# Performance work log

Measured on AMD Instinct MI355X. Metric: run time of the kernel, lower is better.

Reference implementation:

```python
import jax, jax.numpy as jnp
import numpy as np

B, M, C, D, H, W = 2, 4, 32, 32, 32, 32
E, O = 4, 128
MC = M * C
BN_EPS = 1e-5


def setup_inputs() -> dict:
    key = jax.random.key(0)
    ks = jax.random.split(key, 8)
    inp = {
        "f0": jax.random.normal(ks[0], (B, C, D, H, W), jnp.float32),
        "f1": jax.random.normal(ks[1], (B, C, D, H, W), jnp.float32),
        "f2": jax.random.normal(ks[2], (B, C, D, H, W), jnp.float32),
        "f3": jax.random.normal(ks[3], (B, C, D, H, W), jnp.float32),
        # per-expert 1x1x1 conv weights [E, O, MC] (bias=False)
        "Wc": jax.random.normal(ks[4], (E, O, MC), jnp.float32) * 0.05,
        # BatchNorm3d params (eval mode), per expert per out-channel
        "gamma": jnp.ones((E, O), jnp.float32),
        "beta": jnp.zeros((E, O), jnp.float32),
        "rmean": jnp.zeros((E, O), jnp.float32),
        "rvar": jnp.ones((E, O), jnp.float32),
        # router Linear(MC -> E)
        "Wr": jax.random.normal(ks[5], (E, MC), jnp.float32) * 0.02,
        "br": jnp.zeros((E,), jnp.float32),
        "top_k": 2,
    }
    return inp


def reference(f0, f1, f2, f3, Wc, gamma, beta, rmean, rvar, Wr, br, top_k):
    x = jnp.concatenate([f0, f1, f2, f3], axis=1)          # [B, MC, D, H, W]
    Bn, MCn, Dn, Hn, Wn = x.shape
    En = Wr.shape[0]

    # router: global average pool -> linear -> softmax -> top-k
    pooled = x.mean(axis=(2, 3, 4))                        # [B, MC]
    logits = pooled @ Wr.T + br                            # [B, E]
    probs = jax.nn.softmax(logits, axis=-1)
    topk_vals, topk_idx = jax.lax.top_k(probs, top_k)      # [B, k]
    topk_w = topk_vals / topk_vals.sum(axis=-1, keepdims=True)

    # auxiliary load-balancing loss (top-1 one-hot)
    one_hot = jax.nn.one_hot(topk_idx[:, 0], En, dtype=probs.dtype)
    f_e = one_hot.mean(axis=0)
    p_e = probs.mean(axis=0)
    aux_loss = En * (f_e * p_e).sum()

    # all experts: 1x1x1 conv == channel GEMM, then eval-mode BN + ReLU
    xs = x.reshape(Bn, MCn, -1)                            # [B, MC, S]
    y = jnp.einsum('eoc,bcs->ebos', Wc, xs)                # [E, B, O, S]
    inv = gamma * jax.lax.rsqrt(rvar + BN_EPS)             # [E, O]
    y = y * inv[:, None, :, None] + (beta - rmean * inv)[:, None, :, None]
    y = jax.nn.relu(y)

    # dispatch/combine: per-sample expert weights scattered to [B, E]
    cw = jnp.zeros((Bn, En), x.dtype).at[
        jnp.arange(Bn)[:, None], topk_idx
    ].add(topk_w)
    out = jnp.einsum('be,ebos->bos', cw, y).reshape(Bn, -1, Dn, Hn, Wn)
    return out, aux_loss
```

## Files before the change

### kernel.cpp

```cpp
#include <hip/hip_runtime.h>
#include <stdint.h>

#define S_TOT 32768
#define MC_DIM 128
#define O_DIM 128
#define BN_EPS 1e-5f
#define S_TILE 128

#define WS_PART  0
#define WS_BIAS  512
#define WS_W2    1024

typedef __attribute__((ext_vector_type(8))) short short8;
typedef __attribute__((ext_vector_type(4))) float f32x4;

static __device__ __forceinline__ unsigned short f2bf(float f) {
    union { float f; unsigned int u; } v; v.f = f;
    unsigned int r = v.u + 0x7FFFu + ((v.u >> 16) & 1u);
    return (unsigned short)(r >> 16);
}

__global__ __launch_bounds__(256) void k_pool(
    const float* __restrict__ f0, const float* __restrict__ f1,
    const float* __restrict__ f2, const float* __restrict__ f3,
    const float* __restrict__ Wc, const float* __restrict__ gamma,
    const float* __restrict__ beta, const float* __restrict__ rmean,
    const float* __restrict__ rvar, float* __restrict__ ws) {

    __shared__ float red[4];
    int bid = blockIdx.x;
    int b = bid >> 7, c = bid & 127;
    int t = threadIdx.x;
    int wv = t >> 6, l = t & 63;

    if (t < 64) {
        int i = bid * 64 + t;
        int eo = i >> 5;
        float inv = gamma[eo] * rsqrtf(rvar[eo] + BN_EPS);
        float4 w = ((const float4*)Wc)[i];
        uint2 pk;
        pk.x = (unsigned int)f2bf(w.x * inv) | ((unsigned int)f2bf(w.y * inv) << 16);
        pk.y = (unsigned int)f2bf(w.z * inv) | ((unsigned int)f2bf(w.w * inv) << 16);
        ((uint2*)(ws + WS_W2))[i] = pk;
    } else if (t < 66) {
        int i = bid * 2 + (t - 64);
        float inv = gamma[i] * rsqrtf(rvar[i] + BN_EPS);
        ws[WS_BIAS + i] = beta[i] - rmean[i] * inv;
    }

    const float* fp = (c < 32) ? f0 : (c < 64) ? f1 : (c < 96) ? f2 : f3;
    const float4* base = (const float4*)(fp + ((size_t)b * 32 + (c & 31)) * S_TOT);
    float s = 0.f;
    #pragma unroll
    for (int j = 0; j < 32; ++j) {
        float4 v = base[j * 256 + t];
        s += (v.x + v.y) + (v.z + v.w);
    }
    #pragma unroll
    for (int msk = 32; msk >= 1; msk >>= 1) s += __shfl_xor(s, msk);
    if (l == 0) red[wv] = s;
    __syncthreads();
    if (t == 0) ws[WS_PART + bid] = (red[0] + red[1]) + (red[2] + red[3]);
}

__global__ __launch_bounds__(256, 2) void k_moe(
    const float* __restrict__ f0, const float* __restrict__ f1,
    const float* __restrict__ f2, const float* __restrict__ f3,
    const float* __restrict__ Wr, const float* __restrict__ br,
    const float* __restrict__ ws, float* __restrict__ out) {

    __shared__ uint4 tile4[2048];
    char* lds = (char*)tile4;

    int bid = blockIdx.x;
    int b = bid >> 8;
    int st = bid & 255;
    int s0 = st * S_TILE;
    int t = threadIdx.x;
    int wv = t >> 6, l = t & 63;

    float lg[8];
    {
        float p0 = ws[WS_PART + l];
        float p1 = ws[WS_PART + 64 + l];
        float p2 = ws[WS_PART + 128 + l];
        float p3 = ws[WS_PART + 192 + l];
        #pragma unroll
        for (int e = 0; e < 4; ++e) {
            float wc0 = Wr[e * MC_DIM + l];
            float wc1 = Wr[e * MC_DIM + 64 + l];
            lg[e]     = p0 * wc0 + p1 * wc1;
            lg[4 + e] = p2 * wc0 + p3 * wc1;
        }
        #pragma unroll
        for (int msk = 32; msk >= 1; msk >>= 1) {
            #pragma unroll
            for (int e = 0; e < 8; ++e) lg[e] += __shfl_xor(lg[e], msk);
        }
    }
    int e0, e1;
    float w0, w1;
    {
        const float s_inv = 1.0f / (float)S_TOT;
        float probs[2][4];
        int top1[2];
        int ee0[2], ee1[2];
        float vv0[2], vv1[2];
        #pragma unroll
        for (int bb = 0; bb < 2; ++bb) {
            float lo[4];
            #pragma unroll
            for (int e = 0; e < 4; ++e) lo[e] = lg[bb * 4 + e] * s_inv + br[e];
            float mx = fmaxf(fmaxf(lo[0], lo[1]), fmaxf(lo[2], lo[3]));
            float sum = 0.f;
            #pragma unroll
            for (int e = 0; e < 4; ++e) { probs[bb][e] = __expf(lo[e] - mx); sum += probs[bb][e]; }
            float rs = 1.f / sum;
            #pragma unroll
            for (int e = 0; e < 4; ++e) probs[bb][e] *= rs;
            int a0 = 0; float m0 = probs[bb][0];
            #pragma unroll
            for (int e = 1; e < 4; ++e) if (probs[bb][e] > m0) { m0 = probs[bb][e]; a0 = e; }
            int a1 = -1; float m1 = -1.f;
            #pragma unroll
            for (int e = 0; e < 4; ++e) if (e != a0 && probs[bb][e] > m1) { m1 = probs[bb][e]; a1 = e; }
            top1[bb] = a0; ee0[bb] = a0; ee1[bb] = a1; vv0[bb] = m0; vv1[bb] = m1;
        }
        float inv = 1.f / (vv0[b] + vv1[b]);
        e0 = ee0[b]; e1 = ee1[b];
        w0 = vv0[b] * inv; w1 = vv1[b] * inv;
        if (bid == 0 && t == 0) {
            float aux = 0.f;
            #pragma unroll
            for (int e = 0; e < 4; ++e) {
                float fe = 0.5f * ((top1[0] == e) + (top1[1] == e));
                float pe = 0.5f * (probs[0][e] + probs[1][e]);
                aux += fe * pe;
            }
            out[(size_t)8388608] = 4.f * aux;
        }
    }

    #pragma unroll
    for (int m = 0; m < 4; ++m) {
        const float* fp = (m == 0) ? f0 : (m == 1) ? f1 : (m == 2) ? f2 : f3;
        #pragma unroll
        for (int it = 0; it < 4; ++it) {
            int lin = it * 256 + t;
            int cql = lin >> 7;
            int sl = lin & 127;
            const float* src = fp + ((size_t)b * 32 + cql * 4) * S_TOT + s0 + sl;
            float v0 = src[0];
            float v1 = src[S_TOT];
            float v2 = src[2 * (size_t)S_TOT];
            float v3 = src[3 * (size_t)S_TOT];
            int cq = m * 8 + cql;
            int gr = cq >> 1, half = cq & 1;
            int gswz = gr ^ (sl & 15);
            int byte = sl * 256 + gswz * 16 + half * 8;
            uint2 pk;
            pk.x = (unsigned int)f2bf(v0) | ((unsigned int)f2bf(v1) << 16);
            pk.y = (unsigned int)f2bf(v2) | ((unsigned int)f2bf(v3) << 16);
            *(uint2*)(lds + byte) = pk;
        }
    }
    __syncthreads();

    const unsigned short* W2 = (const unsigned short*)(ws + WS_W2);
    const float* bias2 = ws + WS_BIAS;

    int o0 = wv * 32;
    int lr = l & 15, lg2 = l >> 4;

    f32x4 acc[2][2][8];
    #pragma unroll
    for (int ee = 0; ee < 2; ++ee)
        #pragma unroll
        for (int of = 0; of < 2; ++of)
            #pragma unroll
            for (int sf = 0; sf < 8; ++sf)
                acc[ee][of][sf] = (f32x4){0.f, 0.f, 0.f, 0.f};

    #pragma unroll
    for (int kk = 0; kk < 4; ++kk) {
        short8 a[2][2];
        #pragma unroll
        for (int ee = 0; ee < 2; ++ee) {
            int e = ee ? e1 : e0;
            #pragma unroll
            for (int of = 0; of < 2; ++of) {
                int o = o0 + of * 16 + lr;
                a[ee][of] = *(const short8*)(W2 + ((size_t)(e * O_DIM + o) * MC_DIM + kk * 32 + lg2 * 8));
            }
        }
        #pragma unroll
        for (int sf = 0; sf < 8; ++sf) {
            int sl = sf * 16 + lr;
            int gr = kk * 4 + lg2;
            int byte = sl * 256 + ((gr ^ lr) << 4);
            short8 bb = *(const short8*)(lds + byte);
            #pragma unroll
            for (int ee = 0; ee < 2; ++ee)
                #pragma unroll
                for (int of = 0; of < 2; ++of)
                    acc[ee][of][sf] = __builtin_amdgcn_mfma_f32_16x16x32_bf16(
                        a[ee][of], bb, acc[ee][of][sf], 0, 0, 0);
        }
    }

    #pragma unroll
    for (int of = 0; of < 2; ++of) {
        #pragma unroll
        for (int r = 0; r < 4; ++r) {
            int o = o0 + of * 16 + lg2 * 4 + r;
            float bA = bias2[e0 * O_DIM + o];
            float bB = bias2[e1 * O_DIM + o];
            float* orow = out + ((size_t)(b * O_DIM + o)) * S_TOT + s0;
            #pragma unroll
            for (int sf = 0; sf < 8; ++sf) {
                float y0 = fmaxf(acc[0][of][sf][r] + bA, 0.f);
                float y1 = fmaxf(acc[1][of][sf][r] + bB, 0.f);
                orow[sf * 16 + lr] = w0 * y0 + w1 * y1;
            }
        }
    }
}

extern "C" void kernel_launch(void* const* d_in, const int* in_sizes, int n_in,
                              void* d_out, int out_size, void* d_ws, size_t ws_size,
                              hipStream_t stream) {
    const float* f0    = (const float*)d_in[0];
    const float* f1    = (const float*)d_in[1];
    const float* f2    = (const float*)d_in[2];
    const float* f3    = (const float*)d_in[3];
    const float* Wc    = (const float*)d_in[4];
    const float* gamma = (const float*)d_in[5];
    const float* beta  = (const float*)d_in[6];
    const float* rmean = (const float*)d_in[7];
    const float* rvar  = (const float*)d_in[8];
    const float* Wr    = (const float*)d_in[9];
    const float* br    = (const float*)d_in[10];
    float* ws  = (float*)d_ws;
    float* out = (float*)d_out;

    hipLaunchKernelGGL(k_pool, dim3(256), dim3(256), 0, stream,
                       f0, f1, f2, f3, Wc, gamma, beta, rmean, rvar, ws);
    hipLaunchKernelGGL(k_moe, dim3(512), dim3(256), 0, stream,
                       f0, f1, f2, f3, Wr, br, ws, out);
}
```

Baseline: 27.95 us.

## Split pooling across two halves and use 256-wide spatial tiles with 512 threads

The pooling kernel now splits each channel's spatial reduction across two blocks (512 blocks in total), and the MoE kernel sums the two partial results. The MoE kernel doubles its spatial tile to 256 and uses 512-thread blocks in which each wave owns 16 output channels instead of 32, halving the grid to 256 blocks. The aim is more parallelism in the bandwidth-bound pool pass and fewer, larger GEMM blocks that reuse the weight fragments over more spatial columns. In exchange, LDS doubles to 64KB per block and the grid drops to 256 blocks, which may leave CUs idle or lower occupancy.

```diff
diff --git a/kernel.cpp b/kernel.cpp
--- a/kernel.cpp
+++ b/kernel.cpp
@@ -5,7 +5,7 @@
 #define MC_DIM 128
 #define O_DIM 128
 #define BN_EPS 1e-5f
-#define S_TILE 128
+#define S_TILE 256
 
 #define WS_PART  0
 #define WS_BIAS  512
@@ -29,12 +29,13 @@
 
     __shared__ float red[4];
     int bid = blockIdx.x;
-    int b = bid >> 7, c = bid & 127;
+    int half = bid >> 8, ch = bid & 255;
+    int b = ch >> 7, c = ch & 127;
     int t = threadIdx.x;
     int wv = t >> 6, l = t & 63;
 
-    if (t < 64) {
-        int i = bid * 64 + t;
+    if (t < 32) {
+        int i = bid * 32 + t;
         int eo = i >> 5;
         float inv = gamma[eo] * rsqrtf(rvar[eo] + BN_EPS);
         float4 w = ((const float4*)Wc)[i];
@@ -42,17 +43,16 @@
         pk.x = (unsigned int)f2bf(w.x * inv) | ((unsigned int)f2bf(w.y * inv) << 16);
         pk.y = (unsigned int)f2bf(w.z * inv) | ((unsigned int)f2bf(w.w * inv) << 16);
         ((uint2*)(ws + WS_W2))[i] = pk;
-    } else if (t < 66) {
-        int i = bid * 2 + (t - 64);
-        float inv = gamma[i] * rsqrtf(rvar[i] + BN_EPS);
-        ws[WS_BIAS + i] = beta[i] - rmean[i] * inv;
+    } else if (t == 32) {
+        float inv = gamma[bid] * rsqrtf(rvar[bid] + BN_EPS);
+        ws[WS_BIAS + bid] = beta[bid] - rmean[bid] * inv;
     }
 
     const float* fp = (c < 32) ? f0 : (c < 64) ? f1 : (c < 96) ? f2 : f3;
-    const float4* base = (const float4*)(fp + ((size_t)b * 32 + (c & 31)) * S_TOT);
+    const float4* base = (const float4*)(fp + ((size_t)b * 32 + (c & 31)) * S_TOT + half * 16384);
     float s = 0.f;
     #pragma unroll
-    for (int j = 0; j < 32; ++j) {
+    for (int j = 0; j < 16; ++j) {
         float4 v = base[j * 256 + t];
         s += (v.x + v.y) + (v.z + v.w);
     }
@@ -60,31 +60,31 @@
     for (int msk = 32; msk >= 1; msk >>= 1) s += __shfl_xor(s, msk);
     if (l == 0) red[wv] = s;
     __syncthreads();
-    if (t == 0) ws[WS_PART + bid] = (red[0] + red[1]) + (red[2] + red[3]);
-}
-
-__global__ __launch_bounds__(256, 2) void k_moe(
+    if (t == 0) ws[WS_PART + half * 256 + ch] = (red[0] + red[1]) + (red[2] + red[3]);
+}
+
+__global__ __launch_bounds__(512, 1) void k_moe(
     const float* __restrict__ f0, const float* __restrict__ f1,
     const float* __restrict__ f2, const float* __restrict__ f3,
     const float* __restrict__ Wr, const float* __restrict__ br,
     const float* __restrict__ ws, float* __restrict__ out) {
 
-    __shared__ uint4 tile4[2048];
+    __shared__ uint4 tile4[4096];
     char* lds = (char*)tile4;
 
     int bid = blockIdx.x;
-    int b = bid >> 8;
-    int st = bid & 255;
+    int b = bid >> 7;
+    int st = bid & 127;
     int s0 = st * S_TILE;
     int t = threadIdx.x;
     int wv = t >> 6, l = t & 63;
 
     float lg[8];
     {
-        float p0 = ws[WS_PART + l];
-        float p1 = ws[WS_PART + 64 + l];
-        float p2 = ws[WS_PART + 128 + l];
-        float p3 = ws[WS_PART + 192 + l];
+        float p0 = ws[WS_PART + l]       + ws[WS_PART + 256 + l];
+        float p1 = ws[WS_PART + 64 + l]  + ws[WS_PART + 320 + l];
+        float p2 = ws[WS_PART + 128 + l] + ws[WS_PART + 384 + l];
+        float p3 = ws[WS_PART + 192 + l] + ws[WS_PART + 448 + l];
         #pragma unroll
         for (int e = 0; e < 4; ++e) {
             float wc0 = Wr[e * MC_DIM + l];
@@ -146,9 +146,9 @@
         const float* fp = (m == 0) ? f0 : (m == 1) ? f1 : (m == 2) ? f2 : f3;
         #pragma unroll
         for (int it = 0; it < 4; ++it) {
-            int lin = it * 256 + t;
-            int cql = lin >> 7;
-            int sl = lin & 127;
+            int lin = it * 512 + t;
+            int cql = lin >> 8;
+            int sl = lin & 255;
             const float* src = fp + ((size_t)b * 32 + cql * 4) * S_TOT + s0 + sl;
             float v0 = src[0];
             float v1 = src[S_TOT];
@@ -169,59 +169,49 @@
     const unsigned short* W2 = (const unsigned short*)(ws + WS_W2);
     const float* bias2 = ws + WS_BIAS;
 
-    int o0 = wv * 32;
+    int o0 = wv * 16;
     int lr = l & 15, lg2 = l >> 4;
 
-    f32x4 acc[2][2][8];
+    f32x4 acc[2][16];
     #pragma unroll
     for (int ee = 0; ee < 2; ++ee)
         #pragma unroll
-        for (int of = 0; of < 2; ++of)
-            #pragma unroll
-            for (int sf = 0; sf < 8; ++sf)
-                acc[ee][of][sf] = (f32x4){0.f, 0.f, 0.f, 0.f};
+        for (int sf = 0; sf < 16; ++sf)
+            acc[ee][sf] = (f32x4){0.f, 0.f, 0.f, 0.f};
 
     #pragma unroll
     for (int kk = 0; kk < 4; ++kk) {
-        short8 a[2][2];
+        short8 a[2];
         #pragma unroll
         for (int ee = 0; ee < 2; ++ee) {
             int e = ee ? e1 : e0;
-            #pragma unroll
-            for (int of = 0; of < 2; ++of) {
-                int o = o0 + of * 16 + lr;
-                a[ee][of] = *(const short8*)(W2 + ((size_t)(e * O_DIM + o) * MC_DIM + kk * 32 + lg2 * 8));
-            }
-        }
-        #pragma unroll
-        for (int sf = 0; sf < 8; ++sf) {
+            int o = o0 + lr;
+            a[ee] = *(const short8*)(W2 + ((size_t)(e * O_DIM + o) * MC_DIM + kk * 32 + lg2 * 8));
+        }
+        #pragma unroll
+        for (int sf = 0; sf < 16; ++sf) {
             int sl = sf * 16 + lr;
             int gr = kk * 4 + lg2;
             int byte = sl * 256 + ((gr ^ lr) << 4);
             short8 bb = *(const short8*)(lds + byte);
             #pragma unroll
             for (int ee = 0; ee < 2; ++ee)
-                #pragma unroll
-                for (int of = 0; of < 2; ++of)
-                    acc[ee][of][sf] = __builtin_amdgcn_mfma_f32_16x16x32_bf16(
-                        a[ee][of], bb, acc[ee][of][sf], 0, 0, 0);
-        }
-    }
-
-    #pragma unroll
-    for (int of = 0; of < 2; ++of) {
-        #pragma unroll
-        for (int r = 0; r < 4; ++r) {
-            int o = o0 + of * 16 + lg2 * 4 + r;
-            float bA = bias2[e0 * O_DIM + o];
-            float bB = bias2[e1 * O_DIM + o];
-            float* orow = out + ((size_t)(b * O_DIM + o)) * S_TOT + s0;
-            #pragma unroll
-            for (int sf = 0; sf < 8; ++sf) {
-                float y0 = fmaxf(acc[0][of][sf][r] + bA, 0.f);
-                float y1 = fmaxf(acc[1][of][sf][r] + bB, 0.f);
-                orow[sf * 16 + lr] = w0 * y0 + w1 * y1;
-            }
+                acc[ee][sf] = __builtin_amdgcn_mfma_f32_16x16x32_bf16(
+                    a[ee], bb, acc[ee][sf], 0, 0, 0);
+        }
+    }
+
+    #pragma unroll
+    for (int r = 0; r < 4; ++r) {
+        int o = o0 + lg2 * 4 + r;
+        float bA = bias2[e0 * O_DIM + o];
+        float bB = bias2[e1 * O_DIM + o];
+        float* orow = out + ((size_t)(b * O_DIM + o)) * S_TOT + s0;
+        #pragma unroll
+        for (int sf = 0; sf < 16; ++sf) {
+            float y0 = fmaxf(acc[0][sf][r] + bA, 0.f);
+            float y1 = fmaxf(acc[1][sf][r] + bB, 0.f);
+            orow[sf * 16 + lr] = w0 * y0 + w1 * y1;
         }
     }
 }
@@ -243,8 +233,8 @@
     float* ws  = (float*)d_ws;
     float* out = (float*)d_out;
 
-    hipLaunchKernelGGL(k_pool, dim3(256), dim3(256), 0, stream,
+    hipLaunchKernelGGL(k_pool, dim3(512), dim3(256), 0, stream,
                        f0, f1, f2, f3, Wc, gamma, beta, rmean, rvar, ws);
-    hipLaunchKernelGGL(k_moe, dim3(512), dim3(256), 0, stream,
+    hipLaunchKernelGGL(k_moe, dim3(256), dim3(512), 0, stream,
                        f0, f1, f2, f3, Wr, br, ws, out);
 }
```

Measured after the change: 28.35 us. Within noise of the previous version (+1.4%).

## Fuse pooling into MoE kernel with grid-wide flag barrier

Applied to the files above, without the earlier changes.

Merges the separate pooling kernel into the main MoE kernel. Each block now computes partial channel sums from the tile it already loads into LDS and atomically accumulates them into workspace. A software grid barrier built on per-block flags then lets every block compute the router from the completed pool. This removes the second full read of the input and one kernel launch. In exchange it adds a memset, atomics and a spin-wait barrier that depends on all 512 blocks being co-resident, with a deadlock risk if they are not.

```diff
diff --git a/kernel.cpp b/kernel.cpp
--- a/kernel.cpp
+++ b/kernel.cpp
@@ -7,9 +7,10 @@
 #define BN_EPS 1e-5f
 #define S_TILE 128
 
-#define WS_PART  0
-#define WS_BIAS  512
-#define WS_W2    1024
+#define WS_PART2 0
+#define WS_FLAGS 8192
+#define WS_BIAS  12288
+#define WS_W2    12800
 
 typedef __attribute__((ext_vector_type(8))) short short8;
 typedef __attribute__((ext_vector_type(4))) float f32x4;
@@ -20,21 +21,29 @@
     return (unsigned short)(r >> 16);
 }
 
-__global__ __launch_bounds__(256) void k_pool(
+__global__ __launch_bounds__(256, 2) void k_all(
     const float* __restrict__ f0, const float* __restrict__ f1,
     const float* __restrict__ f2, const float* __restrict__ f3,
     const float* __restrict__ Wc, const float* __restrict__ gamma,
     const float* __restrict__ beta, const float* __restrict__ rmean,
-    const float* __restrict__ rvar, float* __restrict__ ws) {
-
-    __shared__ float red[4];
+    const float* __restrict__ rvar, const float* __restrict__ Wr,
+    const float* __restrict__ br, float* __restrict__ ws,
+    float* __restrict__ out) {
+
+    __shared__ uint4 tile4[2048];
+    __shared__ float lds_pool[2][128];
+    __shared__ float pooled_lds[256];
+    char* lds = (char*)tile4;
+
     int bid = blockIdx.x;
-    int b = bid >> 7, c = bid & 127;
+    int b = bid >> 8;
+    int st = bid & 255;
+    int s0 = st * S_TILE;
     int t = threadIdx.x;
     int wv = t >> 6, l = t & 63;
 
-    if (t < 64) {
-        int i = bid * 64 + t;
+    if (t < 32) {
+        int i = bid * 32 + t;
         int eo = i >> 5;
         float inv = gamma[eo] * rsqrtf(rvar[eo] + BN_EPS);
         float4 w = ((const float4*)Wc)[i];
@@ -42,103 +51,9 @@
         pk.x = (unsigned int)f2bf(w.x * inv) | ((unsigned int)f2bf(w.y * inv) << 16);
         pk.y = (unsigned int)f2bf(w.z * inv) | ((unsigned int)f2bf(w.w * inv) << 16);
         ((uint2*)(ws + WS_W2))[i] = pk;
-    } else if (t < 66) {
-        int i = bid * 2 + (t - 64);
-        float inv = gamma[i] * rsqrtf(rvar[i] + BN_EPS);
-        ws[WS_BIAS + i] = beta[i] - rmean[i] * inv;
-    }
-
-    const float* fp = (c < 32) ? f0 : (c < 64) ? f1 : (c < 96) ? f2 : f3;
-    const float4* base = (const float4*)(fp + ((size_t)b * 32 + (c & 31)) * S_TOT);
-    float s = 0.f;
-    #pragma unroll
-    for (int j = 0; j < 32; ++j) {
-        float4 v = base[j * 256 + t];
-        s += (v.x + v.y) + (v.z + v.w);
-    }
-    #pragma unroll
-    for (int msk = 32; msk >= 1; msk >>= 1) s += __shfl_xor(s, msk);
-    if (l == 0) red[wv] = s;
-    __syncthreads();
-    if (t == 0) ws[WS_PART + bid] = (red[0] + red[1]) + (red[2] + red[3]);
-}
-
-__global__ __launch_bounds__(256, 2) void k_moe(
-    const float* __restrict__ f0, const float* __restrict__ f1,
-    const float* __restrict__ f2, const float* __restrict__ f3,
-    const float* __restrict__ Wr, const float* __restrict__ br,
-    const float* __restrict__ ws, float* __restrict__ out) {
-
-    __shared__ uint4 tile4[2048];
-    char* lds = (char*)tile4;
-
-    int bid = blockIdx.x;
-    int b = bid >> 8;
-    int st = bid & 255;
-    int s0 = st * S_TILE;
-    int t = threadIdx.x;
-    int wv = t >> 6, l = t & 63;
-
-    float lg[8];
-    {
-        float p0 = ws[WS_PART + l];
-        float p1 = ws[WS_PART + 64 + l];
-        float p2 = ws[WS_PART + 128 + l];
-        float p3 = ws[WS_PART + 192 + l];
-        #pragma unroll
-        for (int e = 0; e < 4; ++e) {
-            float wc0 = Wr[e * MC_DIM + l];
-            float wc1 = Wr[e * MC_DIM + 64 + l];
-            lg[e]     = p0 * wc0 + p1 * wc1;
-            lg[4 + e] = p2 * wc0 + p3 * wc1;
-        }
-        #pragma unroll
-        for (int msk = 32; msk >= 1; msk >>= 1) {
-            #pragma unroll
-            for (int e = 0; e < 8; ++e) lg[e] += __shfl_xor(lg[e], msk);
-        }
-    }
-    int e0, e1;
-    float w0, w1;
-    {
-        const float s_inv = 1.0f / (float)S_TOT;
-        float probs[2][4];
-        int top1[2];
-        int ee0[2], ee1[2];
-        float vv0[2], vv1[2];
-        #pragma unroll
-        for (int bb = 0; bb < 2; ++bb) {
-            float lo[4];
-            #pragma unroll
-            for (int e = 0; e < 4; ++e) lo[e] = lg[bb * 4 + e] * s_inv + br[e];
-            float mx = fmaxf(fmaxf(lo[0], lo[1]), fmaxf(lo[2], lo[3]));
-            float sum = 0.f;
-            #pragma unroll
-            for (int e = 0; e < 4; ++e) { probs[bb][e] = __expf(lo[e] - mx); sum += probs[bb][e]; }
-            float rs = 1.f / sum;
-            #pragma unroll
-            for (int e = 0; e < 4; ++e) probs[bb][e] *= rs;
-            int a0 = 0; float m0 = probs[bb][0];
-            #pragma unroll
-            for (int e = 1; e < 4; ++e) if (probs[bb][e] > m0) { m0 = probs[bb][e]; a0 = e; }
-            int a1 = -1; float m1 = -1.f;
-            #pragma unroll
-            for (int e = 0; e < 4; ++e) if (e != a0 && probs[bb][e] > m1) { m1 = probs[bb][e]; a1 = e; }
-            top1[bb] = a0; ee0[bb] = a0; ee1[bb] = a1; vv0[bb] = m0; vv1[bb] = m1;
-        }
-        float inv = 1.f / (vv0[b] + vv1[b]);
-        e0 = ee0[b]; e1 = ee1[b];
-        w0 = vv0[b] * inv; w1 = vv1[b] * inv;
-        if (bid == 0 && t == 0) {
-            float aux = 0.f;
-            #pragma unroll
-            for (int e = 0; e < 4; ++e) {
-                float fe = 0.5f * ((top1[0] == e) + (top1[1] == e));
-                float pe = 0.5f * (probs[0][e] + probs[1][e]);
-                aux += fe * pe;
-            }
-            out[(size_t)8388608] = 4.f * aux;
-        }
+    } else if (t == 32) {
+        float inv = gamma[bid] * rsqrtf(rvar[bid] + BN_EPS);
+        ws[WS_BIAS + bid] = beta[bid] - rmean[bid] * inv;
     }
 
     #pragma unroll
@@ -162,9 +77,112 @@
             pk.x = (unsigned int)f2bf(v0) | ((unsigned int)f2bf(v1) << 16);
             pk.y = (unsigned int)f2bf(v2) | ((unsigned int)f2bf(v3) << 16);
             *(uint2*)(lds + byte) = pk;
+            float p0 = v0, p1 = v1, p2 = v2, p3 = v3;
+            #pragma unroll
+            for (int msk = 32; msk >= 1; msk >>= 1) {
+                p0 += __shfl_xor(p0, msk);
+                p1 += __shfl_xor(p1, msk);
+                p2 += __shfl_xor(p2, msk);
+                p3 += __shfl_xor(p3, msk);
+            }
+            if (l == 0) {
+                int c = m * 32 + cql * 4;
+                lds_pool[wv & 1][c + 0] = p0;
+                lds_pool[wv & 1][c + 1] = p1;
+                lds_pool[wv & 1][c + 2] = p2;
+                lds_pool[wv & 1][c + 3] = p3;
+            }
         }
     }
     __syncthreads();
+
+    if (t < 128)
+        atomicAdd(&ws[WS_PART2 + ((b * 32 + (st >> 3)) * 128) + t], lds_pool[0][t] + lds_pool[1][t]);
+
+    {
+        int* flags = (int*)ws + WS_FLAGS;
+        __threadfence();
+        __syncthreads();
+        if (t == 0)
+            __hip_atomic_store(&flags[bid * 8], 1, __ATOMIC_RELEASE, __HIP_MEMORY_SCOPE_AGENT);
+        for (;;) {
+            int v0 = __hip_atomic_load(&flags[t * 8],          __ATOMIC_RELAXED, __HIP_MEMORY_SCOPE_AGENT);
+            int v1 = __hip_atomic_load(&flags[(t + 256) * 8],  __ATOMIC_RELAXED, __HIP_MEMORY_SCOPE_AGENT);
+            if (__syncthreads_and(v0 && v1)) break;
+            __builtin_amdgcn_s_sleep(8);
+        }
+        __threadfence();
+    }
+
+    {
+        int bb = t >> 7, c = t & 127;
+        float s = 0.f;
+        #pragma unroll
+        for (int g = 0; g < 32; ++g)
+            s += ws[WS_PART2 + ((bb * 32 + g) * 128) + c];
+        pooled_lds[t] = s;
+    }
+    __syncthreads();
+
+    int e0, e1;
+    float w0, w1;
+    {
+        float lg[8];
+        float p0 = pooled_lds[l];
+        float p1 = pooled_lds[64 + l];
+        float p2 = pooled_lds[128 + l];
+        float p3 = pooled_lds[192 + l];
+        #pragma unroll
+        for (int e = 0; e < 4; ++e) {
+            float wc0 = Wr[e * MC_DIM + l];
+            float wc1 = Wr[e * MC_DIM + 64 + l];
+            lg[e]     = p0 * wc0 + p1 * wc1;
+            lg[4 + e] = p2 * wc0 + p3 * wc1;
+        }
+        #pragma unroll
+        for (int msk = 32; msk >= 1; msk >>= 1) {
+            #pragma unroll
+            for (int e = 0; e < 8; ++e) lg[e] += __shfl_xor(lg[e], msk);
+        }
+        const float s_inv = 1.0f / (float)S_TOT;
+        float probs[2][4];
+        int top1[2];
+        int ee0[2], ee1[2];
+        float vv0[2], vv1[2];
+        #pragma unroll
+        for (int bb = 0; bb < 2; ++bb) {
+            float lo[4];
+            #pragma unroll
+            for (int e = 0; e < 4; ++e) lo[e] = lg[bb * 4 + e] * s_inv + br[e];
+            float mx = fmaxf(fmaxf(lo[0], lo[1]), fmaxf(lo[2], lo[3]));
+            float sum = 0.f;
+            #pragma unroll
+            for (int e = 0; e < 4; ++e) { probs[bb][e] = __expf(lo[e] - mx); sum += probs[bb][e]; }
+            float rs = 1.f / sum;
+            #pragma unroll
+            for (int e = 0; e < 4; ++e) probs[bb][e] *= rs;
+            int a0 = 0; float m0 = probs[bb][0];
+            #pragma unroll
+            for (int e = 1; e < 4; ++e) if (probs[bb][e] > m0) { m0 = probs[bb][e]; a0 = e; }
+            int a1 = -1; float m1 = -1.f;
+            #pragma unroll
+            for (int e = 0; e < 4; ++e) if (e != a0 && probs[bb][e] > m1) { m1 = probs[bb][e]; a1 = e; }
+            top1[bb] = a0; ee0[bb] = a0; ee1[bb] = a1; vv0[bb] = m0; vv1[bb] = m1;
+        }
+        float inv = 1.f / (vv0[b] + vv1[b]);
+        e0 = ee0[b]; e1 = ee1[b];
+        w0 = vv0[b] * inv; w1 = vv1[b] * inv;
+        if (bid == 0 && t == 0) {
+            float aux = 0.f;
+            #pragma unroll
+            for (int e = 0; e < 4; ++e) {
+                float fe = 0.5f * ((top1[0] == e) + (top1[1] == e));
+                float pe = 0.5f * (probs[0][e] + probs[1][e]);
+                aux += fe * pe;
+            }
+            out[(size_t)8388608] = 4.f * aux;
+        }
+    }
 
     const unsigned short* W2 = (const unsigned short*)(ws + WS_W2);
     const float* bias2 = ws + WS_BIAS;
@@ -243,8 +261,7 @@
     float* ws  = (float*)d_ws;
     float* out = (float*)d_out;
 
-    hipLaunchKernelGGL(k_pool, dim3(256), dim3(256), 0, stream,
-                       f0, f1, f2, f3, Wc, gamma, beta, rmean, rvar, ws);
-    hipLaunchKernelGGL(k_moe, dim3(512), dim3(256), 0, stream,
-                       f0, f1, f2, f3, Wr, br, ws, out);
+    hipMemsetAsync(d_ws, 0, (8192 + 4096) * sizeof(float), stream);
+    hipLaunchKernelGGL(k_all, dim3(512), dim3(256), 0, stream,
+                       f0, f1, f2, f3, Wc, gamma, beta, rmean, rvar, Wr, br, ws, out);
 }
```

Measured after the change: 106.3 us. 280% more time.
